# Kernel tuning notes

Measured on AMD Instinct MI355X. Metric: run time of the kernel, lower is better.

The kernel has to match this reference:

```python
import jax, jax.numpy as jnp
import numpy as np

NUM_LAYERS = 24
LN_EPS = 1e-5


def setup_inputs() -> dict:
    key = jax.random.key(0)
    ks = jax.random.split(key, 8)
    B, S = 256, 8192
    x = jax.random.uniform(ks[0], (B, S, 5), dtype=jnp.float32)
    # per-layer LayerNorm(4) params (torch default init: weight=1, bias=0; use
    # randomized values so the gather is non-trivial)
    ln_w = 1.0 + 0.1 * jax.random.normal(ks[1], (NUM_LAYERS, 4), dtype=jnp.float32)
    ln_b = 0.1 * jax.random.normal(ks[2], (NUM_LAYERS, 4), dtype=jnp.float32)
    # MLP 5 -> 64 -> 32 -> 1 (dropout inactive in eval mode)
    W1 = jax.random.normal(ks[3], (64, 5), dtype=jnp.float32) / np.sqrt(5)
    b1 = jnp.zeros((64,), dtype=jnp.float32)
    W2 = jax.random.normal(ks[4], (32, 64), dtype=jnp.float32) / np.sqrt(64)
    b2 = jnp.zeros((32,), dtype=jnp.float32)
    W3 = jax.random.normal(ks[5], (1, 32), dtype=jnp.float32) / np.sqrt(32)
    b3 = jnp.zeros((1,), dtype=jnp.float32)
    return {"x": x, "ln_w": ln_w, "ln_b": ln_b, "W1": W1, "b1": b1,
            "W2": W2, "b2": b2, "W3": W3, "b3": b3}


def reference(x, ln_w, ln_b, W1, b1, W2, b2, W3, b3):
    B, S, _ = x.shape
    x_flat = x.reshape(-1, 5)                      # [N, 5]
    layer_pos = x_flat[:, -1]                      # [N]
    layer_ids = jnp.clip((layer_pos * NUM_LAYERS).astype(jnp.int32), 0, NUM_LAYERS - 1)
    feats = x_flat[:, :4]                          # [N, 4]
    # vectorized per-token LayerNorm: gather per-token gamma/beta by layer id
    mean = jnp.mean(feats, axis=-1, keepdims=True)
    var = jnp.mean(jnp.square(feats - mean), axis=-1, keepdims=True)  # biased, as torch LN
    normed = (feats - mean) * jax.lax.rsqrt(var + LN_EPS)
    normed = normed * ln_w[layer_ids] + ln_b[layer_ids]               # [N, 4]
    x_norm = jnp.concatenate([normed, layer_pos[:, None]], axis=1)    # [N, 5]
    h = jax.nn.relu(x_norm @ W1.T + b1)            # [N, 64]
    h = jax.nn.relu(h @ W2.T + b2)                 # [N, 32]
    scores = h @ W3.T + b3                         # [N, 1]
    return scores.reshape(B, S)
```

## Files before the change

kernel.cpp:

```cpp
#include <hip/hip_runtime.h>
#include <hip/hip_bf16.h>
#include <stdint.h>

#define NUM_LAYERS 24
#define LN_EPS 1e-5f
#define N_ROWS (256 * 8192)
#define ROWS_PER_ITER 64
#define NUM_ITERS (N_ROWS / ROWS_PER_ITER)
#define NUM_BLOCKS 2048

typedef __attribute__((ext_vector_type(4)))  uint32_t u32x4;
typedef __attribute__((ext_vector_type(16))) float    f32x16;
typedef __attribute__((ext_vector_type(2)))  float    f32x2;
typedef __attribute__((ext_vector_type(2)))  __fp16   h16x2;

__device__ __forceinline__ uint32_t pk_f16_rtz(float lo, float hi) {
    h16x2 v = __builtin_amdgcn_cvt_pkrtz(lo, hi);
    uint32_t u; __builtin_memcpy(&u, &v, 4);
    return u;
}
__device__ __forceinline__ uint32_t pk_f16_rne(float lo, float hi) {
    __fp16 a = (__fp16)lo, b = (__fp16)hi;
    uint16_t ua, ub;
    __builtin_memcpy(&ua, &a, 2); __builtin_memcpy(&ub, &b, 2);
    return (uint32_t)ua | ((uint32_t)ub << 16);
}
__device__ __forceinline__ uint32_t pk_relu_f16(uint32_t d) {
    h16x2 v; __builtin_memcpy(&v, &d, 4);
    h16x2 z = {(__fp16)0.0f, (__fp16)0.0f};
    v = __builtin_elementwise_max(v, z);
    uint32_t u; __builtin_memcpy(&u, &v, 4);
    return u;
}

__device__ __forceinline__ u32x4 make_frag(uint32_t d0, uint32_t d1,
                                           uint32_t d2, uint32_t d3) {
    u32x4 f; f.x = d0; f.y = d1; f.z = d2; f.w = d3;
    return f;
}

__device__ __forceinline__ f32x16 mfma_f16_c(u32x4 a, u32x4 b, const f32x16& c) {
    f32x16 d;
    asm("s_nop 2\n\tv_mfma_f32_32x32x16_f16 %0, %1, %2, %3"
        : "=&v"(d) : "v"(a), "v"(b), "v"(c));
    return d;
}
__device__ __forceinline__ f32x16 mfma_f16_z(u32x4 a, u32x4 b) {
    f32x16 d;
    asm("s_nop 2\n\tv_mfma_f32_32x32x16_f16 %0, %1, %2, 0"
        : "=&v"(d) : "v"(a), "v"(b));
    return d;
}
__device__ __forceinline__ void mfma_f16_acc(f32x16& c, u32x4 a, u32x4 b) {
    asm("s_nop 2\n\tv_mfma_f32_32x32x16_f16 %0, %1, %2, %0"
        : "+v"(c) : "v"(a), "v"(b));
}
__device__ __forceinline__ void mfma_fence2(f32x16& c0, f32x16& c1) {
    asm volatile("s_nop 7\n\ts_nop 7\n\ts_nop 7" : "+v"(c0), "+v"(c1));
}

__device__ __forceinline__ int sigma_k(int p) {
    int hh = (p >> 2) & 1;
    int base = (p & 31) - 4 * hh;
    int r = (base & 3) + 4 * (base >> 3);
    return 32 * (p >> 5) + 16 * (r >> 3) + 8 * hh + (r & 7);
}

__global__ __launch_bounds__(256, 4) void router_mfma(
    const float* __restrict__ x,
    const float* __restrict__ ln_w,
    const float* __restrict__ ln_b,
    const float* __restrict__ W1,
    const float* __restrict__ b1,
    const float* __restrict__ W2,
    const float* __restrict__ b2,
    const float* __restrict__ W3,
    const float* __restrict__ b3,
    float* __restrict__ out)
{
    __shared__ float s_ln[NUM_LAYERS * 8];
    const int t = threadIdx.x;
    if (t < NUM_LAYERS * 4) {
        int lid = t >> 2, c = t & 3;
        s_ln[lid * 8 + c]     = ln_w[t];
        s_ln[lid * 8 + 4 + c] = ln_b[t];
    }
    __syncthreads();

    const int lane = t & 63;
    const int wid  = t >> 6;
    const int n32  = lane & 31;
    const int h    = lane >> 5;

    u32x4 a1f[2];
#pragma unroll
    for (int mt = 0; mt < 2; ++mt) {
        int p = mt * 32 + n32;
        int k = sigma_k(p);
        uint32_t d0 = pk_f16_rne(W1[k * 5 + 0], W1[k * 5 + 1]);
        uint32_t d1 = pk_f16_rne(W1[k * 5 + 2], W1[k * 5 + 3]);
        uint32_t d2 = pk_f16_rne(W1[k * 5 + 4], b1[k]);
        if (h) { d0 = 0; d1 = 0; d2 = 0; }
        a1f[mt] = make_frag(d0, d1, d2, 0);
    }

    u32x4 w2f[4];
#pragma unroll
    for (int kt = 0; kt < 4; ++kt) {
        const float* wp = W2 + n32 * 64 + kt * 16 + h * 8;
        const float4 lo = *(const float4*)(wp);
        const float4 hi = *(const float4*)(wp + 4);
        w2f[kt] = make_frag(pk_f16_rne(lo.x, lo.y), pk_f16_rne(lo.z, lo.w),
                            pk_f16_rne(hi.x, hi.y), pk_f16_rne(hi.z, hi.w));
    }

    f32x16 c2init;
    f32x2 w3p[8];
#pragma unroll
    for (int r2 = 0; r2 < 8; ++r2) {
        const int n = ((2 * r2) & 3) + 8 * (r2 >> 1) + 4 * h;
        w3p[r2] = f32x2{W3[n], W3[n + 1]};
        c2init[2 * r2]     = b2[n];
        c2init[2 * r2 + 1] = b2[n + 1];
    }
    const float b3v = b3[0];
    const f32x2 z2 = {0.0f, 0.0f};

    const int total_waves = NUM_BLOCKS * 4;
    const int w = blockIdx.x * 4 + wid;

    int it = w;
    const float* xp0 = x + (size_t)(it * ROWS_PER_ITER + lane) * 5;
    float f0 = xp0[0], f1 = xp0[1], f2 = xp0[2], f3 = xp0[3], lp = xp0[4];

    while (true) {
        const int nit = it + total_waves;
        const bool more = nit < NUM_ITERS;
        const float* nxp =
            x + (size_t)((more ? nit : it) * ROWS_PER_ITER + lane) * 5;
        const float nf0 = nxp[0], nf1 = nxp[1], nf2 = nxp[2], nf3 = nxp[3],
                    nlp = nxp[4];

        const int rowBase = it * ROWS_PER_ITER;

        int lid = (int)(lp * (float)NUM_LAYERS);
        lid = lid < 0 ? 0 : (lid > NUM_LAYERS - 1 ? NUM_LAYERS - 1 : lid);

        const float m  = (f0 + f1 + f2 + f3) * 0.25f;
        const float d0 = f0 - m, d1 = f1 - m, d2 = f2 - m, d3 = f3 - m;
        const float var = (d0 * d0 + d1 * d1 + d2 * d2 + d3 * d3) * 0.25f;
        const float r   = rsqrtf(var + LN_EPS);

        const float4 g  = *(const float4*)(s_ln + lid * 8);
        const float4 bb = *(const float4*)(s_ln + lid * 8 + 4);

        const float xn0 = fmaf(d0 * r, g.x, bb.x);
        const float xn1 = fmaf(d1 * r, g.y, bb.y);
        const float xn2 = fmaf(d2 * r, g.z, bb.z);
        const float xn3 = fmaf(d3 * r, g.w, bb.w);

        const uint32_t e0 = pk_f16_rtz(xn0, xn1);
        const uint32_t e1 = pk_f16_rtz(xn2, xn3);
        const uint32_t e2 = pk_f16_rtz(lp, 1.0f);
        const uint32_t x0 = __shfl_xor((int)e0, 32, 64);
        const uint32_t x1 = __shfl_xor((int)e1, 32, 64);
        const uint32_t x2 = __shfl_xor((int)e2, 32, 64);

        const u32x4 bf_t0 = make_frag(e0, e1, e2, 0u);
        const u32x4 bf_t1 = make_frag(x0, x1, x2, 0u);

        float res[2];
#pragma unroll
        for (int tile = 0; tile < 2; ++tile) {
            const u32x4 b1f = tile ? bf_t1 : bf_t0;

            f32x16 c1a = mfma_f16_z(a1f[0], b1f);
            f32x16 c1b = mfma_f16_z(a1f[1], b1f);
            mfma_fence2(c1a, c1b);

            u32x4 h1f[4];
#pragma unroll
            for (int kt = 0; kt < 4; ++kt) {
                const f32x16& c1 = (kt < 2) ? c1a : c1b;
                const int roff = 8 * (kt & 1);
                uint32_t dw[4];
#pragma unroll
                for (int d = 0; d < 4; ++d)
                    dw[d] = pk_relu_f16(
                        pk_f16_rtz(c1[roff + 2 * d], c1[roff + 2 * d + 1]));
                h1f[kt] = make_frag(dw[0], dw[1], dw[2], dw[3]);
            }

            f32x16 c2a = mfma_f16_c(w2f[0], h1f[0], c2init);
            f32x16 c2b = mfma_f16_z(w2f[1], h1f[1]);
            mfma_f16_acc(c2a, w2f[2], h1f[2]);
            mfma_f16_acc(c2b, w2f[3], h1f[3]);
            mfma_fence2(c2a, c2b);

            f32x2 acc = z2;
#pragma unroll
            for (int r2 = 0; r2 < 8; ++r2) {
                f32x2 v = {c2a[2 * r2] + c2b[2 * r2],
                           c2a[2 * r2 + 1] + c2b[2 * r2 + 1]};
                v = __builtin_elementwise_max(v, z2);
                acc = v * w3p[r2] + acc;
            }
            float part = acc.x + acc.y;
            part += __shfl_xor(part, 32, 64);
            res[tile] = part;
        }

        out[rowBase + lane] = (h ? res[1] : res[0]) + b3v;

        if (!more) break;
        it = nit;
        f0 = nf0; f1 = nf1; f2 = nf2; f3 = nf3; lp = nlp;
    }
}

extern "C" void kernel_launch(void* const* d_in, const int* in_sizes, int n_in,
                              void* d_out, int out_size, void* d_ws, size_t ws_size,
                              hipStream_t stream) {
    const float* x    = (const float*)d_in[0];
    const float* ln_w = (const float*)d_in[1];
    const float* ln_b = (const float*)d_in[2];
    const float* W1   = (const float*)d_in[3];
    const float* b1   = (const float*)d_in[4];
    const float* W2   = (const float*)d_in[5];
    const float* b2   = (const float*)d_in[6];
    const float* W3   = (const float*)d_in[7];
    const float* b3   = (const float*)d_in[8];
    float* out = (float*)d_out;

    router_mfma<<<NUM_BLOCKS, 256, 0, stream>>>(x, ln_w, ln_b, W1, b1, W2, b2,
                                                W3, b3, out);
}
```

Before: 110.2 us.

## Interleave both MFMA tiles per iteration and lower occupancy to three blocks

Issues the layer-1 and layer-2 MFMAs for both 32-row tiles together, so independent matrix ops fill each other's latency. It uses one accumulator chain per tile instead of two partial accumulators per tile. Register use grows, so launch bounds drop to 3 blocks per SM and the persistent grid shrinks to 768 blocks. The risk is that lower occupancy hides memory latency less well.

```diff
diff --git a/kernel.cpp b/kernel.cpp
--- a/kernel.cpp
+++ b/kernel.cpp
@@ -7,7 +7,7 @@
 #define N_ROWS (256 * 8192)
 #define ROWS_PER_ITER 64
 #define NUM_ITERS (N_ROWS / ROWS_PER_ITER)
-#define NUM_BLOCKS 2048
+#define NUM_BLOCKS 768
 
 typedef __attribute__((ext_vector_type(4)))  uint32_t u32x4;
 typedef __attribute__((ext_vector_type(16))) float    f32x16;
@@ -58,6 +58,11 @@
 __device__ __forceinline__ void mfma_fence2(f32x16& c0, f32x16& c1) {
     asm volatile("s_nop 7\n\ts_nop 7\n\ts_nop 7" : "+v"(c0), "+v"(c1));
 }
+__device__ __forceinline__ void mfma_fence4(f32x16& c0, f32x16& c1,
+                                            f32x16& c2, f32x16& c3) {
+    asm volatile("s_nop 7\n\ts_nop 7\n\ts_nop 7"
+                 : "+v"(c0), "+v"(c1), "+v"(c2), "+v"(c3));
+}
 
 __device__ __forceinline__ int sigma_k(int p) {
     int hh = (p >> 2) & 1;
@@ -66,7 +71,7 @@
     return 32 * (p >> 5) + 16 * (r >> 3) + 8 * hh + (r & 7);
 }
 
-__global__ __launch_bounds__(256, 4) void router_mfma(
+__global__ __launch_bounds__(256, 3) void router_mfma(
     const float* __restrict__ x,
     const float* __restrict__ ln_w,
     const float* __restrict__ ln_b,
@@ -169,48 +174,61 @@
         const u32x4 bf_t0 = make_frag(e0, e1, e2, 0u);
         const u32x4 bf_t1 = make_frag(x0, x1, x2, 0u);
 
-        float res[2];
-#pragma unroll
-        for (int tile = 0; tile < 2; ++tile) {
-            const u32x4 b1f = tile ? bf_t1 : bf_t0;
-
-            f32x16 c1a = mfma_f16_z(a1f[0], b1f);
-            f32x16 c1b = mfma_f16_z(a1f[1], b1f);
-            mfma_fence2(c1a, c1b);
-
-            u32x4 h1f[4];
-#pragma unroll
-            for (int kt = 0; kt < 4; ++kt) {
-                const f32x16& c1 = (kt < 2) ? c1a : c1b;
-                const int roff = 8 * (kt & 1);
-                uint32_t dw[4];
-#pragma unroll
-                for (int d = 0; d < 4; ++d)
-                    dw[d] = pk_relu_f16(
-                        pk_f16_rtz(c1[roff + 2 * d], c1[roff + 2 * d + 1]));
-                h1f[kt] = make_frag(dw[0], dw[1], dw[2], dw[3]);
-            }
-
-            f32x16 c2a = mfma_f16_c(w2f[0], h1f[0], c2init);
-            f32x16 c2b = mfma_f16_z(w2f[1], h1f[1]);
-            mfma_f16_acc(c2a, w2f[2], h1f[2]);
-            mfma_f16_acc(c2b, w2f[3], h1f[3]);
-            mfma_fence2(c2a, c2b);
-
-            f32x2 acc = z2;
-#pragma unroll
-            for (int r2 = 0; r2 < 8; ++r2) {
-                f32x2 v = {c2a[2 * r2] + c2b[2 * r2],
-                           c2a[2 * r2 + 1] + c2b[2 * r2 + 1]};
-                v = __builtin_elementwise_max(v, z2);
-                acc = v * w3p[r2] + acc;
-            }
-            float part = acc.x + acc.y;
-            part += __shfl_xor(part, 32, 64);
-            res[tile] = part;
-        }
-
-        out[rowBase + lane] = (h ? res[1] : res[0]) + b3v;
+        f32x16 c1a0 = mfma_f16_z(a1f[0], bf_t0);
+        f32x16 c1b0 = mfma_f16_z(a1f[1], bf_t0);
+        f32x16 c1a1 = mfma_f16_z(a1f[0], bf_t1);
+        f32x16 c1b1 = mfma_f16_z(a1f[1], bf_t1);
+        mfma_fence4(c1a0, c1b0, c1a1, c1b1);
+
+        u32x4 h1f0[4], h1f1[4];
+#pragma unroll
+        for (int kt = 0; kt < 4; ++kt) {
+            const f32x16& c1 = (kt < 2) ? c1a0 : c1b0;
+            const int roff = 8 * (kt & 1);
+            uint32_t dw[4];
+#pragma unroll
+            for (int d = 0; d < 4; ++d)
+                dw[d] = pk_relu_f16(
+                    pk_f16_rtz(c1[roff + 2 * d], c1[roff + 2 * d + 1]));
+            h1f0[kt] = make_frag(dw[0], dw[1], dw[2], dw[3]);
+        }
+#pragma unroll
+        for (int kt = 0; kt < 4; ++kt) {
+            const f32x16& c1 = (kt < 2) ? c1a1 : c1b1;
+            const int roff = 8 * (kt & 1);
+            uint32_t dw[4];
+#pragma unroll
+            for (int d = 0; d < 4; ++d)
+                dw[d] = pk_relu_f16(
+                    pk_f16_rtz(c1[roff + 2 * d], c1[roff + 2 * d + 1]));
+            h1f1[kt] = make_frag(dw[0], dw[1], dw[2], dw[3]);
+        }
+
+        f32x16 c2_0 = mfma_f16_c(w2f[0], h1f0[0], c2init);
+        f32x16 c2_1 = mfma_f16_c(w2f[0], h1f1[0], c2init);
+#pragma unroll
+        for (int kt = 1; kt < 4; ++kt) {
+            mfma_f16_acc(c2_0, w2f[kt], h1f0[kt]);
+            mfma_f16_acc(c2_1, w2f[kt], h1f1[kt]);
+        }
+        mfma_fence2(c2_0, c2_1);
+
+        f32x2 acc0 = z2, acc1 = z2;
+#pragma unroll
+        for (int r2 = 0; r2 < 8; ++r2) {
+            f32x2 v0 = {c2_0[2 * r2], c2_0[2 * r2 + 1]};
+            f32x2 v1 = {c2_1[2 * r2], c2_1[2 * r2 + 1]};
+            v0 = __builtin_elementwise_max(v0, z2);
+            v1 = __builtin_elementwise_max(v1, z2);
+            acc0 = v0 * w3p[r2] + acc0;
+            acc1 = v1 * w3p[r2] + acc1;
+        }
+        float p0 = acc0.x + acc0.y;
+        float p1 = acc1.x + acc1.y;
+        p0 += __shfl_xor(p0, 32, 64);
+        p1 += __shfl_xor(p1, 32, 64);
+
+        out[rowBase + lane] = (h ? p1 : p0) + b3v;
 
         if (!more) break;
         it = nit;
```

After: 108.8 us. No clear change (-1.3%).
